# Performance work log

Hardware: AMD Instinct MI355X
Metric: run time of the kernel (lower is better)

The kernel has to match this reference:

```python
import jax, jax.numpy as jnp
import numpy as np

N_HEAD = 12
LN_EPS = 1e-5


def _layernorm(x, g, b):
    m = jnp.mean(x, axis=-1, keepdims=True)
    v = jnp.mean(jnp.square(x - m), axis=-1, keepdims=True)
    return (x - m) * jax.lax.rsqrt(v + LN_EPS) * g + b


def _block(x, p):
    # p holds single-layer params. x: [B, S, D]
    B, S, D = x.shape
    Dh = D // N_HEAD
    h = _layernorm(x, p['ln1_g'], p['ln1_b'])
    q = (h @ p['wq'] + p['bq']).reshape(B, S, N_HEAD, Dh)
    k = (h @ p['wk'] + p['bk']).reshape(B, S, N_HEAD, Dh)
    v = (h @ p['wv'] + p['bv']).reshape(B, S, N_HEAD, Dh)
    scores = jnp.einsum('bqhd,bkhd->bhqk', q, k) / np.sqrt(Dh).astype(x.dtype)
    causal = jnp.tril(jnp.ones((S, S), dtype=bool))  # valid_nums = arange(1..S)
    scores = jnp.where(causal, scores, -jnp.inf)
    attn = jax.nn.softmax(scores, axis=-1)  # dropout is identity in eval
    o = jnp.einsum('bhqk,bkhd->bqhd', attn, v).reshape(B, S, D)
    x = x + o @ p['wo'] + p['bo']
    h2 = _layernorm(x, p['ln2_g'], p['ln2_b'])
    ff = jax.nn.gelu(h2 @ p['w1'] + p['b1'], approximate=False) @ p['w2'] + p['b2']
    return x + ff


def _gpt_forward(idx, wte, wpe, layer_params, lnf_g, lnf_b, lm_w):
    S = idx.shape[1]
    x = wte[idx] + wpe[None, :S, :]  # embd dropout is identity in eval
    x = jax.lax.scan(lambda c, p: (_block(c, p), None), x, layer_params)[0]
    x = _layernorm(x, lnf_g, lnf_b)
    return x @ lm_w  # logits [B, S, V]


def setup_inputs() -> dict:
    B, S, D, V, L, F = 4, 1024, 768, 50257, 12, 3072
    key = jax.random.key(0)
    ks = iter(jax.random.split(key, 24))
    std = 0.02
    std_proj = 0.02 / np.sqrt(2 * L)  # special init for w_o / FFN.linear2

    def w(shape, s=std):
        return jax.random.normal(next(ks), shape, jnp.float32) * s

    return dict(
        idx=jax.random.randint(next(ks), (B, S), 0, V),
        wte=w((V, D)), wpe=w((S, D)),
        ln1_g=jnp.ones((L, D)), ln1_b=jnp.zeros((L, D)),
        wq=w((L, D, D)), bq=jnp.zeros((L, D)),
        wk=w((L, D, D)), bk=jnp.zeros((L, D)),
        wv=w((L, D, D)), bv=jnp.zeros((L, D)),
        wo=w((L, D, D), std_proj), bo=jnp.zeros((L, D)),
        ln2_g=jnp.ones((L, D)), ln2_b=jnp.zeros((L, D)),
        w1=w((L, D, F)), b1=jnp.zeros((L, F)),
        w2=w((L, F, D), std_proj), b2=jnp.zeros((L, D)),
        lnf_g=jnp.ones((D,)), lnf_b=jnp.zeros((D,)),
        lm_w=w((D, V)),
    )


def reference(idx, wte, wpe, ln1_g, ln1_b, wq, bq, wk, bk, wv, bv, wo, bo,
              ln2_g, ln2_b, w1, b1, w2, b2, lnf_g, lnf_b, lm_w):
    layer_params = dict(ln1_g=ln1_g, ln1_b=ln1_b, wq=wq, bq=bq, wk=wk, bk=bk,
                        wv=wv, bv=bv, wo=wo, bo=bo, ln2_g=ln2_g, ln2_b=ln2_b,
                        w1=w1, b1=b1, w2=w2, b2=b2)
    return _gpt_forward(idx, wte, wpe, layer_params, lnf_g, lnf_b, lm_w)
```

## Files before the change

### kernel.cpp

```cpp
#include <hip/hip_runtime.h>
#include <hip/hip_bf16.h>

typedef __attribute__((ext_vector_type(8))) short short8;
typedef __attribute__((ext_vector_type(4))) short short4v;
typedef __attribute__((ext_vector_type(4))) float floatx4;

#define GLD16(g, l) __builtin_amdgcn_global_load_lds( \
    (__attribute__((address_space(1))) void*)(g),      \
    (__attribute__((address_space(3))) void*)(l), 16, 0, 0)

#define MFMA_BF16(a, b, c) __builtin_amdgcn_mfma_f32_16x16x32_bf16((a), (b), (c), 0, 0, 0)

__device__ __forceinline__ short f2bf(float f) {
  union { __hip_bfloat16 h; short s; } u;
  u.h = __float2bfloat16(f);
  return u.s;
}

__global__ __launch_bounds__(256)
void transpose_convert(const float* __restrict__ in, short* __restrict__ out,
                       const int K, const int N, const size_t inStride,
                       const size_t outStride) {
  in += blockIdx.z * inStride;
  out += blockIdx.z * outStride;
  __shared__ float tile[32][33];
  const int n0 = blockIdx.x * 32;
  const int k0 = blockIdx.y * 32;
  const int tx = threadIdx.x;
  const int ty = threadIdx.y;
#pragma unroll
  for (int i = 0; i < 4; ++i) {
    const int kk = ty + i * 8;
    const int nn = n0 + tx;
    tile[kk][tx] = (nn < N) ? in[(size_t)(k0 + kk) * N + nn] : 0.f;
  }
  __syncthreads();
#pragma unroll
  for (int i = 0; i < 4; ++i) {
    const int nn = ty + i * 8;
    out[(size_t)(n0 + nn) * K + k0 + tx] = f2bf(tile[tx][nn]);
  }
}

__global__ __launch_bounds__(256)
void embed_kernel(const int* __restrict__ idx, const float* __restrict__ wte,
                  const float* __restrict__ wpe, float* __restrict__ x) {
  const int row = blockIdx.x;
  const int tok = idx[row];
  const int s = row & 1023;
  const float* wt = wte + (size_t)tok * 768;
  const float* wp = wpe + (size_t)s * 768;
  float* xr = x + (size_t)row * 768;
  for (int c = threadIdx.x; c < 768; c += 256) xr[c] = wt[c] + wp[c];
}

__global__ __launch_bounds__(256)
void ln_kernel(const float* __restrict__ x, const float* __restrict__ g,
               const float* __restrict__ b, short* __restrict__ out) {
  const int wv = threadIdx.x >> 6, lane = threadIdx.x & 63;
  const int row = blockIdx.x * 4 + wv;
  const float* xr = x + (size_t)row * 768 + lane * 12;
  const float4 a0 = *(const float4*)(xr);
  const float4 a1 = *(const float4*)(xr + 4);
  const float4 a2 = *(const float4*)(xr + 8);
  float v[12] = {a0.x, a0.y, a0.z, a0.w, a1.x, a1.y, a1.z, a1.w,
                 a2.x, a2.y, a2.z, a2.w};
  float s = 0.f;
#pragma unroll
  for (int i = 0; i < 12; ++i) s += v[i];
#pragma unroll
  for (int m = 1; m < 64; m <<= 1) s += __shfl_xor(s, m);
  const float mean = s * (1.0f / 768.0f);
  float q = 0.f;
#pragma unroll
  for (int i = 0; i < 12; ++i) {
    v[i] -= mean;
    q += v[i] * v[i];
  }
#pragma unroll
  for (int m = 1; m < 64; m <<= 1) q += __shfl_xor(q, m);
  const float inv = rsqrtf(q * (1.0f / 768.0f) + 1e-5f);

  const float* gp = g + lane * 12;
  const float* bp = b + lane * 12;
  const float4 g0 = *(const float4*)(gp);
  const float4 g1 = *(const float4*)(gp + 4);
  const float4 g2 = *(const float4*)(gp + 8);
  const float4 b0 = *(const float4*)(bp);
  const float4 b1 = *(const float4*)(bp + 4);
  const float4 b2 = *(const float4*)(bp + 8);
  const float gg[12] = {g0.x, g0.y, g0.z, g0.w, g1.x, g1.y, g1.z, g1.w,
                        g2.x, g2.y, g2.z, g2.w};
  const float bb[12] = {b0.x, b0.y, b0.z, b0.w, b1.x, b1.y, b1.z, b1.w,
                        b2.x, b2.y, b2.z, b2.w};
  short r[12];
#pragma unroll
  for (int i = 0; i < 12; ++i) r[i] = f2bf(v[i] * inv * gg[i] + bb[i]);
  short* orow = out + (size_t)row * 768 + lane * 12;
#pragma unroll
  for (int i = 0; i < 3; ++i)
    *(short4v*)(orow + i * 4) = short4v{r[i * 4], r[i * 4 + 1], r[i * 4 + 2],
                                        r[i * 4 + 3]};
}

enum { EPI_QKV = 0, EPI_RESID = 1, EPI_GELU = 2 };

template <int BM, int BN, int DBUF, int EPI>
__global__ __launch_bounds__(256)
void gemm_kernel(const short* __restrict__ A, const short* __restrict__ Bt,
                 const int K,
                 const float* __restrict__ bias0, const float* __restrict__ bias1,
                 const float* __restrict__ bias2, float* __restrict__ fout,
                 short* __restrict__ bout0, short* __restrict__ bout1,
                 short* __restrict__ bout2) {
  constexpr int MF = BM / 32;
  constexpr int NF = BN / 32;
  __shared__ short sA[DBUF + 1][BM * 64];
  __shared__ short sB[DBUF + 1][BN * 64];
  const int tid = threadIdx.x;
  const int wv = tid >> 6;
  const int lane = tid & 63;
  const int lrow = lane & 15;
  const int lk8 = lane >> 4;
  const int m0 = blockIdx.x * BM;
  const int n0 = blockIdx.y * BN;
  const int wm = (wv >> 1) * (BM / 2);
  const int wn = (wv & 1) * (BN / 2);
  constexpr int MW = BM / 2 / 16;
  constexpr int NW = BN / 2 / 16;

  floatx4 acc[MW][NW];
#pragma unroll
  for (int m = 0; m < MW; ++m)
#pragma unroll
    for (int n = 0; n < NW; ++n) acc[m][n] = {0.f, 0.f, 0.f, 0.f};

  const short* pA[MF];
  const short* pB[NF];
#pragma unroll
  for (int i = 0; i < MF; ++i) {
    const int p = i * 256 + tid;
    const int rr = p >> 3, up = p & 7;
    pA[i] = A + (size_t)(m0 + rr) * K + ((up ^ (rr & 7)) << 3);
  }
#pragma unroll
  for (int i = 0; i < NF; ++i) {
    const int p = i * 256 + tid;
    const int rr = p >> 3, up = p & 7;
    pB[i] = Bt + (size_t)(n0 + rr) * K + ((up ^ (rr & 7)) << 3);
  }

  auto stage = [&](int buf) {
#pragma unroll
    for (int i = 0; i < MF; ++i) {
      GLD16(pA[i], sA[buf] + (i * 256 + wv * 64) * 8);
      pA[i] += 64;
    }
#pragma unroll
    for (int i = 0; i < NF; ++i) {
      GLD16(pB[i], sB[buf] + (i * 256 + wv * 64) * 8);
      pB[i] += 64;
    }
  };

  auto compute = [&](const short* pa, const short* pb) {
    const int xr = lrow & 7;
    short8 af[MW][2], bv[NW][2];
#pragma unroll
    for (int m = 0; m < MW; ++m) {
      const int row = (wm + m * 16 + lrow) * 64;
      af[m][0] = *(const short8*)(pa + row + ((lk8 ^ xr) << 3));
      af[m][1] = *(const short8*)(pa + row + (((4 + lk8) ^ xr) << 3));
    }
#pragma unroll
    for (int n = 0; n < NW; ++n) {
      const int row = (wn + n * 16 + lrow) * 64;
      bv[n][0] = *(const short8*)(pb + row + ((lk8 ^ xr) << 3));
      bv[n][1] = *(const short8*)(pb + row + (((4 + lk8) ^ xr) << 3));
    }
#pragma unroll
    for (int m = 0; m < MW; ++m)
#pragma unroll
      for (int n = 0; n < NW; ++n) {
        acc[m][n] = MFMA_BF16(af[m][0], bv[n][0], acc[m][n]);
        acc[m][n] = MFMA_BF16(af[m][1], bv[n][1], acc[m][n]);
      }
  };

  const int nk = K >> 6;
  if (DBUF) {
    stage(0);
    __syncthreads();
    int cur = 0;
    for (int kt = 0; kt < nk; ++kt) {
      if (kt + 1 < nk) stage(cur ^ 1);
      compute(sA[cur], sB[cur]);
      __syncthreads();
      cur ^= 1;
    }
  } else {
    for (int kt = 0; kt < nk; ++kt) {
      stage(0);
      __syncthreads();
      compute(sA[0], sB[0]);
      __syncthreads();
    }
  }

#pragma unroll
  for (int m = 0; m < MW; ++m) {
#pragma unroll
    for (int n = 0; n < NW; ++n) {
#pragma unroll
      for (int r = 0; r < 4; ++r) {
        const float v = acc[m][n][r];
        const int gm = m0 + wm + m * 16 + lk8 * 4 + r;
        const int gn = n0 + wn + n * 16 + lrow;
        if (EPI == EPI_QKV) {
          const int sec = (gn >= 1536) ? 2 : (gn >= 768 ? 1 : 0);
          const int nn = gn - sec * 768;
          const int hh = nn >> 6, dh = nn & 63;
          const int bb = gm >> 10, srow = gm & 1023;
          if (sec == 0) {
            bout0[(((size_t)(bb * 12 + hh) * 1024 + srow) << 6) + dh] =
                f2bf((v + bias0[nn]) * 0.18033688f);
          } else if (sec == 1) {
            bout1[(((size_t)(bb * 12 + hh) * 1024 + srow) << 6) + dh] =
                f2bf(v + bias1[nn]);
          } else {
            bout2[(((size_t)(bb * 12 + hh) * 64 + dh) << 10) + srow] =
                f2bf(v + bias2[nn]);
          }
        } else if (EPI == EPI_RESID) {
          float* xp = fout + (size_t)gm * 768 + gn;
          *xp = *xp + v + bias0[gn];
        } else {
          const float tt = v + bias0[gn];
          const float gl = 0.5f * tt * (1.f + erff(tt * 0.70710678118654752f));
          bout0[(size_t)gm * 3072 + gn] = f2bf(gl);
        }
      }
    }
  }
}

__global__ __launch_bounds__(512, 4)
void gemm_lm_kernel(const short* __restrict__ A, const short* __restrict__ Bt,
                    float* __restrict__ fout) {
  __shared__ short sA[256 * 64];
  __shared__ short sB[128 * 64];
  const int K = 768;
  const int tid = threadIdx.x;
  const int wv = tid >> 6;
  const int lane = tid & 63;
  const int lrow = lane & 15;
  const int lk8 = lane >> 4;
  const int m0 = blockIdx.x * 256;
  const int n0 = blockIdx.y * 128;
  const int wm = (wv >> 1) * 64;
  const int wn = (wv & 1) * 64;

  floatx4 acc[4][4];
#pragma unroll
  for (int m = 0; m < 4; ++m)
#pragma unroll
    for (int n = 0; n < 4; ++n) acc[m][n] = {0.f, 0.f, 0.f, 0.f};

  const short* Ab = A + (size_t)m0 * K;
  const short* Bb = Bt + (size_t)n0 * K;

  const short* pA[4];
  const short* pB[2];
#pragma unroll
  for (int i = 0; i < 4; ++i) {
    const int p = i * 512 + tid;
    const int rr = p >> 3, up = p & 7;
    pA[i] = Ab + (size_t)rr * K + ((up ^ (rr & 7)) << 3);
  }
#pragma unroll
  for (int i = 0; i < 2; ++i) {
    const int p = i * 512 + tid;
    const int rr = p >> 3, up = p & 7;
    pB[i] = Bb + (size_t)rr * K + ((up ^ (rr & 7)) << 3);
  }

  const int arow = (wm + lrow) * 64;
  const int xr = (lrow & 7);

  for (int kt = 0; kt < 12; ++kt) {
#pragma unroll
    for (int i = 0; i < 4; ++i) {
      GLD16(pA[i], sA + (i * 512 + wv * 64) * 8);
      pA[i] += 64;
    }
#pragma unroll
    for (int i = 0; i < 2; ++i) {
      GLD16(pB[i], sB + (i * 512 + wv * 64) * 8);
      pB[i] += 64;
    }
    __syncthreads();

    short8 bvv[4][2];
#pragma unroll
    for (int n = 0; n < 4; ++n) {
      const int brow = (wn + n * 16 + lrow) * 64;
      bvv[n][0] = *(const short8*)(sB + brow + ((lk8 ^ xr) << 3));
      bvv[n][1] = *(const short8*)(sB + brow + (((4 + lk8) ^ xr) << 3));
    }
#pragma unroll
    for (int m = 0; m < 4; ++m) {
      const short8 a0 = *(const short8*)(sA + arow + m * 1024 + ((lk8 ^ xr) << 3));
      const short8 a1 =
          *(const short8*)(sA + arow + m * 1024 + (((4 + lk8) ^ xr) << 3));
#pragma unroll
      for (int n = 0; n < 4; ++n) {
        acc[m][n] = MFMA_BF16(a0, bvv[n][0], acc[m][n]);
        acc[m][n] = MFMA_BF16(a1, bvv[n][1], acc[m][n]);
      }
    }
    __syncthreads();
  }

#pragma unroll
  for (int m = 0; m < 4; ++m)
#pragma unroll
    for (int n = 0; n < 4; ++n)
#pragma unroll
      for (int r = 0; r < 4; ++r) {
        const int gm = m0 + wm + m * 16 + lk8 * 4 + r;
        const int gn = n0 + wn + n * 16 + lrow;
        if (gn < 50257) fout[(size_t)gm * 50257 + gn] = acc[m][n][r];
      }
}

__global__ __launch_bounds__(256)
void attn_kernel(const short* __restrict__ q, const short* __restrict__ k,
                 const short* __restrict__ vt, short* __restrict__ o) {
  __shared__ short sK[2][64 * 64];
  __shared__ short sV[2][64 * 64];
  const int bh = blockIdx.x;
  const int qi = 15 - blockIdx.y;
  const int tid = threadIdx.x;
  const int wv = tid >> 6, lane = tid & 63;
  const int lrow = lane & 15, lk8 = lane >> 4;
  const int q0 = qi * 64;
  const int qrow = q0 + wv * 16 + lrow;

  const short* qg = q + ((size_t)(bh * 1024 + qrow)) * 64 + lk8 * 8;
  const short8 qf0 = *(const short8*)qg;
  const short8 qf1 = *(const short8*)(qg + 32);

  const int e0 = tid * 8, e1 = (256 + tid) * 8;
  const int sr0 = e0 >> 6, sc0 = e0 & 63;
  const int sr1 = e1 >> 6, sc1 = e1 & 63;
  const int su0 = ((sc0 >> 3) ^ (sr0 & 7)) << 3;
  const int su1 = ((sc1 >> 3) ^ (sr1 & 7)) << 3;
  const short* kb = k + (size_t)bh * 1024 * 64;
  const short* vb = vt + (size_t)bh * 64 * 1024;

  short8 kreg0, kreg1, vreg0, vreg1;
  auto load_tile = [&](int k0) {
    kreg0 = *(const short8*)(kb + (size_t)(k0 + sr0) * 64 + sc0);
    kreg1 = *(const short8*)(kb + (size_t)(k0 + sr1) * 64 + sc1);
    vreg0 = *(const short8*)(vb + (size_t)sr0 * 1024 + k0 + sc0);
    vreg1 = *(const short8*)(vb + (size_t)sr1 * 1024 + k0 + sc1);
  };
  auto write_tile = [&](short* dK, short* dV) {
    *(short8*)(dK + sr0 * 64 + su0) = kreg0;
    *(short8*)(dK + sr1 * 64 + su1) = kreg1;
    *(short8*)(dV + sr0 * 64 + su0) = vreg0;
    *(short8*)(dV + sr1 * 64 + su1) = vreg1;
  };

  float m_run = -1e30f, lsum = 0.f;
  floatx4 accO[4];
#pragma unroll
  for (int n = 0; n < 4; ++n) accO[n] = {0.f, 0.f, 0.f, 0.f};

  load_tile(0);
  write_tile(sK[0], sV[0]);
  __syncthreads();

  int cur = 0;
  for (int t = 0; t <= qi; ++t) {
    const int k0 = t * 64;
    if (t < qi) load_tile(k0 + 64);

    floatx4 accS[4];
#pragma unroll
    for (int n = 0; n < 4; ++n) accS[n] = {0.f, 0.f, 0.f, 0.f};
    const int rKb = ((lrow >> 2) << 3) + (lrow & 3);
    const short* pK = sK[cur];
    const short* pV = sV[cur];
#pragma unroll
    for (int ks = 0; ks < 2; ++ks) {
      const short8 qf = ks ? qf1 : qf0;
#pragma unroll
      for (int n = 0; n < 4; ++n) {
        const int rK = ((n >> 1) << 5) + ((n & 1) << 2) + rKb;
        const short8 kf =
            *(const short8*)(pK + rK * 64 + (((ks * 4 + lk8) ^ (rK & 7)) << 3));
        accS[n] = MFMA_BF16(kf, qf, accS[n]);
      }
    }

    float sv[4][4];
    float mx = -1e30f;
#pragma unroll
    for (int n = 0; n < 4; ++n)
#pragma unroll
      for (int r = 0; r < 4; ++r) {
        const int key = k0 + ((n >> 1) << 5) + (lk8 << 3) + ((n & 1) << 2) + r;
        float s = accS[n][r];
        s = (key > qrow) ? -1e30f : s;
        sv[n][r] = s;
        mx = fmaxf(mx, s);
      }
    mx = fmaxf(mx, __shfl_xor(mx, 16));
    mx = fmaxf(mx, __shfl_xor(mx, 32));

    const bool skip = __all(mx <= m_run + 8.0f);
    float sf = 1.f;
    if (!skip) {
      const float mnew = fmaxf(m_run, mx);
      sf = exp2f(m_run - mnew);
      m_run = mnew;
    }

    float rs = 0.f;
    unsigned int w[4][2];
#pragma unroll
    for (int n = 0; n < 4; ++n)
#pragma unroll
      for (int rp = 0; rp < 2; ++rp) {
        const float ea = exp2f(sv[n][2 * rp] - m_run);
        const float eb = exp2f(sv[n][2 * rp + 1] - m_run);
        rs += ea + eb;
        w[n][rp] = (unsigned int)(unsigned short)f2bf(ea) |
                   ((unsigned int)(unsigned short)f2bf(eb) << 16);
      }

    if (skip) {
      lsum += rs;
    } else {
      lsum = lsum * sf + rs;
      float sfq[4];
#pragma unroll
      for (int r = 0; r < 4; ++r)
        sfq[r] = __shfl(sf, (lane & 48) | (lk8 * 4 + r));
#pragma unroll
      for (int n = 0; n < 4; ++n)
#pragma unroll
        for (int r = 0; r < 4; ++r) accO[n][r] *= sfq[r];
    }

    union { short8 s; unsigned int u[4]; } paf0, paf1;
#pragma unroll
    for (int tt = 0; tt < 4; ++tt) {
      paf0.u[tt] = w[tt >> 1][tt & 1];
      paf1.u[tt] = w[2 + (tt >> 1)][tt & 1];
    }

#pragma unroll
    for (int n = 0; n < 4; ++n) {
      const int dh = n * 16 + lrow;
      const short8 vf0 = *(const short8*)(pV + dh * 64 + ((lk8 ^ (dh & 7)) << 3));
      const short8 vf1 =
          *(const short8*)(pV + dh * 64 + (((4 + lk8) ^ (dh & 7)) << 3));
      accO[n] = MFMA_BF16(paf0.s, vf0, accO[n]);
      accO[n] = MFMA_BF16(paf1.s, vf1, accO[n]);
    }

    if (t < qi) write_tile(sK[cur ^ 1], sV[cur ^ 1]);
    __syncthreads();
    cur ^= 1;
  }

  float ls = lsum;
  ls += __shfl_xor(ls, 16);
  ls += __shfl_xor(ls, 32);
  const float invown = 1.f / ls;
  float invq[4];
#pragma unroll
  for (int r = 0; r < 4; ++r)
    invq[r] = __shfl(invown, (lane & 48) | (lk8 * 4 + r));

  const int bb = bh / 12, hh = bh % 12;
#pragma unroll
  for (int n = 0; n < 4; ++n)
#pragma unroll
    for (int r = 0; r < 4; ++r) {
      const int row = q0 + wv * 16 + lk8 * 4 + r;
      const float ov = accO[n][r] * invq[r];
      o[((size_t)(bb * 1024 + row)) * 768 + hh * 64 + n * 16 + lrow] = f2bf(ov);
    }
}

extern "C" void kernel_launch(void* const* d_in, const int* in_sizes, int n_in,
                              void* d_out, int out_size, void* d_ws, size_t ws_size,
                              hipStream_t stream) {
  const int* idx = (const int*)d_in[0];
  const float* wte = (const float*)d_in[1];
  const float* wpe = (const float*)d_in[2];
  const float* ln1_g = (const float*)d_in[3];
  const float* ln1_b = (const float*)d_in[4];
  const float* wq = (const float*)d_in[5];
  const float* bq = (const float*)d_in[6];
  const float* wk = (const float*)d_in[7];
  const float* bk = (const float*)d_in[8];
  const float* wv = (const float*)d_in[9];
  const float* bv = (const float*)d_in[10];
  const float* wo = (const float*)d_in[11];
  const float* bo = (const float*)d_in[12];
  const float* ln2_g = (const float*)d_in[13];
  const float* ln2_b = (const float*)d_in[14];
  const float* w1 = (const float*)d_in[15];
  const float* b1 = (const float*)d_in[16];
  const float* w2 = (const float*)d_in[17];
  const float* b2 = (const float*)d_in[18];
  const float* lnf_g = (const float*)d_in[19];
  const float* lnf_b = (const float*)d_in[20];
  const float* lm_w = (const float*)d_in[21];
  float* out = (float*)d_out;

  char* base = (char*)d_ws;
  size_t off = 0;
  auto alloc = [&](size_t bytes) {
    char* r = base + off;
    off = (off + bytes + 255) & ~(size_t)255;
    return r;
  };
  short* lmT = (short*)alloc((size_t)50304 * 768 * 2);
  float* x = (float*)alloc((size_t)4096 * 768 * 4);
  short* h = (short*)alloc((size_t)4096 * 768 * 2);
  short* qb = (short*)alloc((size_t)4096 * 768 * 2);
  short* kb = (short*)alloc((size_t)4096 * 768 * 2);
  short* vtb = (short*)alloc((size_t)4096 * 768 * 2);
  short* ob = (short*)alloc((size_t)4096 * 768 * 2);
  short* ff = (short*)alloc((size_t)4096 * 3072 * 2);

  const size_t LW = 7077888;
  const size_t dd = (size_t)768 * 768;
  const bool big = (off + (size_t)12 * LW * 2 + 256 <= ws_size);
  short* wAll = nullptr;
  short *wqkvT = nullptr, *woT = nullptr, *w1T = nullptr, *w2T = nullptr;
  if (big) {
    wAll = (short*)alloc((size_t)12 * LW * 2);
  } else {
    wqkvT = (short*)alloc((size_t)2304 * 768 * 2);
    woT = (short*)alloc((size_t)768 * 768 * 2);
    w1T = (short*)alloc((size_t)3072 * 768 * 2);
    w2T = (short*)alloc((size_t)768 * 3072 * 2);
    if (off > ws_size) return;
  }

  const dim3 tb(32, 8);
  transpose_convert<<<dim3(1572, 24, 1), tb, 0, stream>>>(lm_w, lmT, 768, 50257, 0, 0);
  if (big) {
    transpose_convert<<<dim3(24, 24, 12), tb, 0, stream>>>(wq, wAll + 0, 768, 768, dd, LW);
    transpose_convert<<<dim3(24, 24, 12), tb, 0, stream>>>(wk, wAll + 589824, 768, 768, dd, LW);
    transpose_convert<<<dim3(24, 24, 12), tb, 0, stream>>>(wv, wAll + 1179648, 768, 768, dd, LW);
    transpose_convert<<<dim3(24, 24, 12), tb, 0, stream>>>(wo, wAll + 1769472, 768, 768, dd, LW);
    transpose_convert<<<dim3(96, 24, 12), tb, 0, stream>>>(w1, wAll + 2359296, 768, 3072,
                                                           (size_t)768 * 3072, LW);
    transpose_convert<<<dim3(24, 96, 12), tb, 0, stream>>>(w2, wAll + 4718592, 3072, 768,
                                                           (size_t)3072 * 768, LW);
  }
  embed_kernel<<<4096, 256, 0, stream>>>(idx, wte, wpe, x);

  for (int l = 0; l < 12; ++l) {
    const short *pQKV, *pWO, *pW1, *pW2;
    if (big) {
      short* wl = wAll + (size_t)l * LW;
      pQKV = wl;
      pWO = wl + 1769472;
      pW1 = wl + 2359296;
      pW2 = wl + 4718592;
    } else {
      transpose_convert<<<dim3(24, 24, 1), tb, 0, stream>>>(wq + l * dd, wqkvT, 768, 768, 0, 0);
      transpose_convert<<<dim3(24, 24, 1), tb, 0, stream>>>(wk + l * dd, wqkvT + dd, 768, 768, 0, 0);
      transpose_convert<<<dim3(24, 24, 1), tb, 0, stream>>>(wv + l * dd, wqkvT + 2 * dd, 768, 768, 0, 0);
      transpose_convert<<<dim3(24, 24, 1), tb, 0, stream>>>(wo + l * dd, woT, 768, 768, 0, 0);
      transpose_convert<<<dim3(96, 24, 1), tb, 0, stream>>>(w1 + (size_t)l * 768 * 3072, w1T, 768, 3072, 0, 0);
      transpose_convert<<<dim3(24, 96, 1), tb, 0, stream>>>(w2 + (size_t)l * 3072 * 768, w2T, 3072, 768, 0, 0);
      pQKV = wqkvT; pWO = woT; pW1 = w1T; pW2 = w2T;
    }

    ln_kernel<<<1024, 256, 0, stream>>>(x, ln1_g + l * 768, ln1_b + l * 768, h);
    gemm_kernel<128, 64, 1, EPI_QKV><<<dim3(32, 36), 256, 0, stream>>>(
        h, pQKV, 768, bq + l * 768, bk + l * 768, bv + l * 768, nullptr, qb, kb, vtb);
    attn_kernel<<<dim3(48, 16), 256, 0, stream>>>(qb, kb, vtb, ob);
    gemm_kernel<64, 64, 1, EPI_RESID><<<dim3(64, 12), 256, 0, stream>>>(
        ob, pWO, 768, bo + l * 768, nullptr, nullptr, x, nullptr, nullptr, nullptr);
    ln_kernel<<<1024, 256, 0, stream>>>(x, ln2_g + l * 768, ln2_b + l * 768, h);
    gemm_kernel<128, 64, 1, EPI_GELU><<<dim3(32, 48), 256, 0, stream>>>(
        h, pW1, 768, b1 + l * 3072, nullptr, nullptr, nullptr, ff, nullptr, nullptr);
    gemm_kernel<64, 64, 1, EPI_RESID><<<dim3(64, 12), 256, 0, stream>>>(
        ff, pW2, 3072, b2 + l * 768, nullptr, nullptr, x, nullptr, nullptr, nullptr);
  }

  ln_kernel<<<1024, 256, 0, stream>>>(x, lnf_g, lnf_b, h);
  gemm_lm_kernel<<<dim3(16, 393), 512, 0, stream>>>(h, lmT, out);
}
```

Before: 2.829 ms.

## Pipeline GEMM global-to-LDS loads with partial vmcnt waits and double-buffer LM head

Replaces the __syncthreads-based double buffering in the layer GEMMs with explicit s_waitcnt vmcnt(N) waits. Only the previous stage's async global_load_lds must complete before the barrier, so the next tile's loads stay in flight during compute. The LM-head GEMM gains a double-buffered LDS pipeline in the same style, which doubles its shared memory, and its occupancy hint drops from 4 to 2 blocks. The MFMA section is wrapped in s_setprio. The hand-counted vmcnt values depend on the number of loads issued per stage, so a miscount would create a race.

```diff
diff --git a/kernel.cpp b/kernel.cpp
--- a/kernel.cpp
+++ b/kernel.cpp
@@ -16,6 +16,14 @@
   u.h = __float2bfloat16(f);
   return u.s;
 }
+
+template <int N>
+__device__ __forceinline__ void wait_vm() {
+  if constexpr (N == 0) asm volatile("s_waitcnt vmcnt(0)" ::: "memory");
+  else if constexpr (N == 4) asm volatile("s_waitcnt vmcnt(4)" ::: "memory");
+  else if constexpr (N == 6) asm volatile("s_waitcnt vmcnt(6)" ::: "memory");
+}
+__device__ __forceinline__ void cfence() { asm volatile("" ::: "memory"); }
 
 __global__ __launch_bounds__(256)
 void transpose_convert(const float* __restrict__ in, short* __restrict__ out,
@@ -105,7 +113,7 @@
 
 enum { EPI_QKV = 0, EPI_RESID = 1, EPI_GELU = 2 };
 
-template <int BM, int BN, int DBUF, int EPI>
+template <int BM, int BN, int EPI>
 __global__ __launch_bounds__(256)
 void gemm_kernel(const short* __restrict__ A, const short* __restrict__ Bt,
                  const int K,
@@ -115,8 +123,9 @@
                  short* __restrict__ bout2) {
   constexpr int MF = BM / 32;
   constexpr int NF = BN / 32;
-  __shared__ short sA[DBUF + 1][BM * 64];
-  __shared__ short sB[DBUF + 1][BN * 64];
+  constexpr int NL = MF + NF;
+  __shared__ short sA[2][BM * 64];
+  __shared__ short sB[2][BN * 64];
   const int tid = threadIdx.x;
   const int wv = tid >> 6;
   const int lane = tid & 63;
@@ -188,23 +197,23 @@
   };
 
   const int nk = K >> 6;
-  if (DBUF) {
-    stage(0);
-    __syncthreads();
-    int cur = 0;
-    for (int kt = 0; kt < nk; ++kt) {
-      if (kt + 1 < nk) stage(cur ^ 1);
-      compute(sA[cur], sB[cur]);
-      __syncthreads();
-      cur ^= 1;
-    }
-  } else {
-    for (int kt = 0; kt < nk; ++kt) {
-      stage(0);
-      __syncthreads();
-      compute(sA[0], sB[0]);
-      __syncthreads();
-    }
+  stage(0);
+  int cur = 0;
+  for (int kt = 0; kt < nk; ++kt) {
+    if (kt + 1 < nk) {
+      stage(cur ^ 1);
+      wait_vm<NL>();
+    } else {
+      wait_vm<0>();
+    }
+    __builtin_amdgcn_s_barrier();
+    cfence();
+    __builtin_amdgcn_s_setprio(1);
+    compute(sA[cur], sB[cur]);
+    __builtin_amdgcn_s_setprio(0);
+    cfence();
+    __builtin_amdgcn_s_barrier();
+    cur ^= 1;
   }
 
 #pragma unroll
@@ -244,11 +253,11 @@
   }
 }
 
-__global__ __launch_bounds__(512, 4)
+__global__ __launch_bounds__(512, 2)
 void gemm_lm_kernel(const short* __restrict__ A, const short* __restrict__ Bt,
                     float* __restrict__ fout) {
-  __shared__ short sA[256 * 64];
-  __shared__ short sB[128 * 64];
+  __shared__ short sA[2][256 * 64];
+  __shared__ short sB[2][128 * 64];
   const int K = 768;
   const int tid = threadIdx.x;
   const int wv = tid >> 6;
@@ -284,41 +293,59 @@
     pB[i] = Bb + (size_t)rr * K + ((up ^ (rr & 7)) << 3);
   }
 
+  auto stage = [&](int buf) {
+#pragma unroll
+    for (int i = 0; i < 4; ++i) {
+      GLD16(pA[i], sA[buf] + (i * 512 + wv * 64) * 8);
+      pA[i] += 64;
+    }
+#pragma unroll
+    for (int i = 0; i < 2; ++i) {
+      GLD16(pB[i], sB[buf] + (i * 512 + wv * 64) * 8);
+      pB[i] += 64;
+    }
+  };
+
   const int arow = (wm + lrow) * 64;
   const int xr = (lrow & 7);
 
+  stage(0);
+  int cur = 0;
   for (int kt = 0; kt < 12; ++kt) {
-#pragma unroll
-    for (int i = 0; i < 4; ++i) {
-      GLD16(pA[i], sA + (i * 512 + wv * 64) * 8);
-      pA[i] += 64;
-    }
-#pragma unroll
-    for (int i = 0; i < 2; ++i) {
-      GLD16(pB[i], sB + (i * 512 + wv * 64) * 8);
-      pB[i] += 64;
-    }
-    __syncthreads();
-
+    if (kt + 1 < 12) {
+      stage(cur ^ 1);
+      wait_vm<6>();
+    } else {
+      wait_vm<0>();
+    }
+    __builtin_amdgcn_s_barrier();
+    cfence();
+
+    const short* pa = sA[cur];
+    const short* pb = sB[cur];
     short8 bvv[4][2];
 #pragma unroll
     for (int n = 0; n < 4; ++n) {
       const int brow = (wn + n * 16 + lrow) * 64;
-      bvv[n][0] = *(const short8*)(sB + brow + ((lk8 ^ xr) << 3));
-      bvv[n][1] = *(const short8*)(sB + brow + (((4 + lk8) ^ xr) << 3));
-    }
+      bvv[n][0] = *(const short8*)(pb + brow + ((lk8 ^ xr) << 3));
+      bvv[n][1] = *(const short8*)(pb + brow + (((4 + lk8) ^ xr) << 3));
+    }
+    __builtin_amdgcn_s_setprio(1);
 #pragma unroll
     for (int m = 0; m < 4; ++m) {
-      const short8 a0 = *(const short8*)(sA + arow + m * 1024 + ((lk8 ^ xr) << 3));
+      const short8 a0 = *(const short8*)(pa + arow + m * 1024 + ((lk8 ^ xr) << 3));
       const short8 a1 =
-          *(const short8*)(sA + arow + m * 1024 + (((4 + lk8) ^ xr) << 3));
+          *(const short8*)(pa + arow + m * 1024 + (((4 + lk8) ^ xr) << 3));
 #pragma unroll
       for (int n = 0; n < 4; ++n) {
         acc[m][n] = MFMA_BF16(a0, bvv[n][0], acc[m][n]);
         acc[m][n] = MFMA_BF16(a1, bvv[n][1], acc[m][n]);
       }
     }
-    __syncthreads();
+    __builtin_amdgcn_s_setprio(0);
+    cfence();
+    __builtin_amdgcn_s_barrier();
+    cur ^= 1;
   }
 
 #pragma unroll
@@ -587,15 +614,15 @@
     }
 
     ln_kernel<<<1024, 256, 0, stream>>>(x, ln1_g + l * 768, ln1_b + l * 768, h);
-    gemm_kernel<128, 64, 1, EPI_QKV><<<dim3(32, 36), 256, 0, stream>>>(
+    gemm_kernel<128, 64, EPI_QKV><<<dim3(32, 36), 256, 0, stream>>>(
         h, pQKV, 768, bq + l * 768, bk + l * 768, bv + l * 768, nullptr, qb, kb, vtb);
     attn_kernel<<<dim3(48, 16), 256, 0, stream>>>(qb, kb, vtb, ob);
-    gemm_kernel<64, 64, 1, EPI_RESID><<<dim3(64, 12), 256, 0, stream>>>(
+    gemm_kernel<64, 64, EPI_RESID><<<dim3(64, 12), 256, 0, stream>>>(
         ob, pWO, 768, bo + l * 768, nullptr, nullptr, x, nullptr, nullptr, nullptr);
     ln_kernel<<<1024, 256, 0, stream>>>(x, ln2_g + l * 768, ln2_b + l * 768, h);
-    gemm_kernel<128, 64, 1, EPI_GELU><<<dim3(32, 48), 256, 0, stream>>>(
+    gemm_kernel<128, 64, EPI_GELU><<<dim3(32, 48), 256, 0, stream>>>(
         h, pW1, 768, b1 + l * 3072, nullptr, nullptr, nullptr, ff, nullptr, nullptr);
-    gemm_kernel<64, 64, 1, EPI_RESID><<<dim3(64, 12), 256, 0, stream>>>(
+    gemm_kernel<64, 64, EPI_RESID><<<dim3(64, 12), 256, 0, stream>>>(
         ff, pW2, 3072, b2 + l * 768, nullptr, nullptr, x, nullptr, nullptr, nullptr);
   }
 
```

After: 2.942 ms. +4.0%, slower.
